# Kernel tuning notes

Measured on AMD Instinct MI355X. Metric: run time of the kernel, lower is better.

The kernel has to match this reference:

```python
import jax, jax.numpy as jnp
import numpy as np

COST_CLASS = 1.0
COST_MASK = 1.0
COST_DICE = 1.0


def setup_inputs() -> dict:
    key = jax.random.key(0)
    k1, k2, k3, k4 = jax.random.split(key, 4)
    B, Q, T, H, W, C = 4, 100, 20, 128, 128, 80
    out_probs = jax.random.normal(k1, (B, Q, C), dtype=jnp.float32)
    out_masks = jax.random.uniform(k2, (B, Q, H, W), dtype=jnp.float32)
    target_masks = jax.random.uniform(k3, (B, T, H, W), dtype=jnp.float32)
    target_labels = jax.random.randint(k4, (B, T), 0, C, dtype=jnp.int64)
    return {"out_probs": out_probs, "out_masks": out_masks,
            "target_masks": target_masks, "target_labels": target_labels}


def reference(out_probs, out_masks, target_masks, target_labels):
    # out_probs: [B,Q,C]; out_masks: [B,Q,H,W]; target_masks: [B,T,H,W]; target_labels: [B,T]
    B, Q = out_probs.shape[:2]
    T = target_labels.shape[1]

    # Classification cost: -softmax(out_probs)[b, q, target_labels[b, t]] -> [B,Q,T]
    prob = jax.nn.softmax(out_probs, axis=-1)
    idx = jnp.broadcast_to(target_labels[:, None, :], (B, Q, T))
    cost_class = -jnp.take_along_axis(prob, idx, axis=2)

    out_flat = out_masks.reshape(B, Q, -1)      # [B,Q,HW]
    tgt_flat = target_masks.reshape(B, T, -1)   # [B,T,HW]

    # Pairwise L1 cost over pixels: [B,Q,T]
    cost_mask = jnp.abs(out_flat[:, :, None, :] - tgt_flat[:, None, :, :]).sum(-1)

    # Pairwise dice cost: numerator via batched matmul, sums broadcast.
    inter = jnp.einsum('bqn,btn->bqt', out_flat, tgt_flat)
    denom = out_flat.sum(-1)[:, :, None] + tgt_flat.sum(-1)[:, None, :]
    cost_dice = 1.0 - (2.0 * inter + 1.0) / (denom + 1.0)

    C_mat = COST_MASK * cost_mask + COST_CLASS * cost_class + COST_DICE * cost_dice
    return C_mat  # [B,Q,T] cost matrix (Hungarian assignment runs on CPU outside)
```

## Files before the change

### kernel.cpp

```cpp
#include <hip/hip_runtime.h>
#include <hip/hip_bf16.h>
#include <math.h>

#define B_ 4
#define Q_ 100
#define T_ 20
#define C_ 80
#define HW_ 16384

#define S_ 16
#define QG_ 4
#define GPB_ (Q_ / QG_)
#define GROUPS_ (B_ * GPB_)
#define SEG4_ (HW_ / S_ / 4)
#define NITER_ (SEG4_ / 64)
#define TW_ 5
#define SUBS_ 4
#define QREC_ 41
#define REC_ (QG_ * QREC_ * SUBS_)
#define GWS_OFF ((size_t)GROUPS_ * S_ * REC_)

typedef float f32x4 __attribute__((ext_vector_type(4)));

__device__ __forceinline__ f32x4 ldnt(const f32x4* p) {
    return __builtin_nontemporal_load(p);
}

__device__ __forceinline__ float wave_reduce4(float v) {
    v += __shfl_down(v, 32);
    v += __shfl_down(v, 16);
    v += __shfl_down(v, 8);
    v += __shfl_down(v, 4);
    return v;
}

template <bool WITH_G>
__device__ __forceinline__ void partial_body(const f32x4* __restrict__ o4,
                                             const f32x4* __restrict__ g4,
                                             float* __restrict__ rec,
                                             float* __restrict__ grec,
                                             int lane, int wave) {
    const int t0 = wave * TW_;

    float accL[QG_][TW_];
    float accI[QG_][TW_];
    float osum[QG_];
    float gsum[TW_];
#pragma unroll
    for (int qi = 0; qi < QG_; ++qi) {
        osum[qi] = 0.f;
#pragma unroll
        for (int tj = 0; tj < TW_; ++tj) { accL[qi][tj] = 0.f; accI[qi][tj] = 0.f; }
    }
#pragma unroll
    for (int tj = 0; tj < TW_; ++tj) gsum[tj] = 0.f;

    const f32x4* op = o4 + lane;
    const f32x4* gp = g4 + (size_t)t0 * (HW_ / 4) + lane;

    f32x4 oc[QG_], gc[TW_], on[QG_], gn[TW_];
#pragma unroll
    for (int qi = 0; qi < QG_; ++qi) oc[qi] = ldnt(op + (size_t)qi * (HW_ / 4));
#pragma unroll
    for (int tj = 0; tj < TW_; ++tj) gc[tj] = gp[(size_t)tj * (HW_ / 4)];

#pragma unroll
    for (int it = 0; it < NITER_; ++it) {
        if (it + 1 < NITER_) {
            const int ofs = (it + 1) * 64;
#pragma unroll
            for (int qi = 0; qi < QG_; ++qi) on[qi] = ldnt(op + (size_t)qi * (HW_ / 4) + ofs);
#pragma unroll
            for (int tj = 0; tj < TW_; ++tj) gn[tj] = gp[(size_t)tj * (HW_ / 4) + ofs];
        }
#pragma unroll
        for (int qi = 0; qi < QG_; ++qi)
            osum[qi] += (oc[qi].x + oc[qi].y) + (oc[qi].z + oc[qi].w);
#pragma unroll
        for (int tj = 0; tj < TW_; ++tj) {
            const f32x4 g = gc[tj];
            if (WITH_G) gsum[tj] += (g.x + g.y) + (g.z + g.w);
#pragma unroll
            for (int qi = 0; qi < QG_; ++qi) {
                const f32x4 o = oc[qi];
                accL[qi][tj] += (fabsf(o.x - g.x) + fabsf(o.y - g.y)) +
                                (fabsf(o.z - g.z) + fabsf(o.w - g.w));
                accI[qi][tj] = fmaf(o.x, g.x, accI[qi][tj]);
                accI[qi][tj] = fmaf(o.y, g.y, accI[qi][tj]);
                accI[qi][tj] = fmaf(o.z, g.z, accI[qi][tj]);
                accI[qi][tj] = fmaf(o.w, g.w, accI[qi][tj]);
            }
        }
        if (it + 1 < NITER_) {
#pragma unroll
            for (int qi = 0; qi < QG_; ++qi) oc[qi] = on[qi];
#pragma unroll
            for (int tj = 0; tj < TW_; ++tj) gc[tj] = gn[tj];
        }
    }

#pragma unroll
    for (int qi = 0; qi < QG_; ++qi) {
#pragma unroll
        for (int tj = 0; tj < TW_; ++tj) {
            const float vL = wave_reduce4(accL[qi][tj]);
            const float vI = wave_reduce4(accI[qi][tj]);
            if (lane < SUBS_) {
                rec[(qi * QREC_ + (t0 + tj)) * SUBS_ + lane]      = vL;
                rec[(qi * QREC_ + 20 + (t0 + tj)) * SUBS_ + lane] = vI;
            }
        }
        const float vo = wave_reduce4(osum[qi]);
        if (wave == 0 && lane < SUBS_) rec[(qi * QREC_ + 40) * SUBS_ + lane] = vo;
    }
    if (WITH_G) {
#pragma unroll
        for (int tj = 0; tj < TW_; ++tj) {
            const float vg = wave_reduce4(gsum[tj]);
            if (lane < SUBS_) grec[(t0 + tj) * SUBS_ + lane] = vg;
        }
    }
}

__global__ __launch_bounds__(256) void partial_kernel(const float* __restrict__ outm,
                                                      const float* __restrict__ tgtm,
                                                      float* __restrict__ ws) {
    const int r = blockIdx.x & 7;
    const int m = blockIdx.x >> 3;
    const int b = r >> 1;
    const int l = m * 2 + (r & 1);
    const int grp_local = l >> 4;
    const int seg = l & (S_ - 1);
    const int qbase = grp_local * QG_;
    const int grp = b * GPB_ + grp_local;

    const int lane = threadIdx.x & 63;
    const int wave = threadIdx.x >> 6;

    const f32x4* o4 = (const f32x4*)(outm + ((size_t)b * Q_ + qbase) * HW_) + seg * SEG4_;
    const f32x4* g4 = (const f32x4*)(tgtm + (size_t)b * T_ * HW_) + seg * SEG4_;
    float* rec  = ws + (size_t)(grp * S_ + seg) * REC_;
    float* grec = ws + GWS_OFF + (size_t)(b * S_ + seg) * T_ * SUBS_;

    if (grp_local == 0) partial_body<true>(o4, g4, rec, grec, lane, wave);
    else                partial_body<false>(o4, g4, rec, grec, lane, wave);
}

__global__ __launch_bounds__(64) void finalize_kernel(const float* __restrict__ probs,
                                                      const int*   __restrict__ labels,
                                                      const float* __restrict__ ws,
                                                      float* __restrict__ out) {
    const int bq = blockIdx.x;
    const int b = bq / Q_;
    const int q = bq % Q_;
    const int grp = b * GPB_ + q / QG_;
    const int qi  = q % QG_;

    __shared__ float s_logit[C_];
    for (int c = threadIdx.x; c < C_; c += 64)
        s_logit[c] = probs[(size_t)bq * C_ + c];
    __syncthreads();

    const int t = threadIdx.x;
    if (t < T_) {
        float L = 0.f, I = 0.f, os = 0.f, ts = 0.f;
#pragma unroll
        for (int s = 0; s < S_; ++s) {
            const float4* r4 = (const float4*)(ws + (size_t)(grp * S_ + s) * REC_);
            const float4* d4 = (const float4*)(ws + GWS_OFF + (size_t)(b * S_ + s) * T_ * SUBS_);
            const float4 a = r4[qi * QREC_ + t];
            const float4 v = r4[qi * QREC_ + 20 + t];
            const float4 c = r4[qi * QREC_ + 40];
            const float4 d = d4[t];
            L  += (a.x + a.y) + (a.z + a.w);
            I  += (v.x + v.y) + (v.z + v.w);
            os += (c.x + c.y) + (c.z + c.w);
            ts += (d.x + d.y) + (d.z + d.w);
        }
        float mx = -INFINITY;
#pragma unroll
        for (int c = 0; c < C_; ++c) mx = fmaxf(mx, s_logit[c]);
        float sum = 0.f;
#pragma unroll
        for (int c = 0; c < C_; ++c) sum += __expf(s_logit[c] - mx);
        const int lab = labels[b * T_ + t];
        const float p = __expf(s_logit[lab] - mx) / sum;

        const float denom = os + ts;
        const float dice = 1.f - (2.f * I + 1.f) / (denom + 1.f);

        out[(size_t)bq * T_ + t] = L - p + dice;
    }
}

extern "C" void kernel_launch(void* const* d_in, const int* in_sizes, int n_in,
                              void* d_out, int out_size, void* d_ws, size_t ws_size,
                              hipStream_t stream) {
    const float* out_probs     = (const float*)d_in[0];
    const float* out_masks     = (const float*)d_in[1];
    const float* target_masks  = (const float*)d_in[2];
    const int*   target_labels = (const int*)d_in[3];
    float* out = (float*)d_out;

    float* partials = (float*)d_ws;

    partial_kernel<<<GROUPS_ * S_, 256, 0, stream>>>(out_masks, target_masks, partials);
    finalize_kernel<<<B_ * Q_, 64, 0, stream>>>(out_probs, target_labels, partials, out);
}
```

Measured before the change: 37.29 us.

## Stage target-mask chunks into double-buffered LDS via global_load_lds

Target-mask tiles are no longer loaded into per-wave registers. They are copied asynchronously straight into a double-buffered shared-memory array with the global_load_lds builtin. Waves stage rows cooperatively and each wave then reads its own 5 rows from LDS. The aim is to cut register pressure from the gc/gn prefetch registers and overlap target fetches with compute. The cost is a block-wide barrier every iteration, plus reliance on the builtin's uniform-LDS-base addressing matching the per-lane destination layout.

```diff
diff --git a/kernel.cpp b/kernel.cpp
--- a/kernel.cpp
+++ b/kernel.cpp
@@ -13,7 +13,8 @@
 #define GPB_ (Q_ / QG_)
 #define GROUPS_ (B_ * GPB_)
 #define SEG4_ (HW_ / S_ / 4)
-#define NITER_ (SEG4_ / 64)
+#define CH_ 64
+#define NITER_ (SEG4_ / CH_)
 #define TW_ 5
 #define SUBS_ 4
 #define QREC_ 41
@@ -24,6 +25,13 @@
 
 __device__ __forceinline__ f32x4 ldnt(const f32x4* p) {
     return __builtin_nontemporal_load(p);
+}
+
+__device__ __forceinline__ void stage16(const f32x4* gsrc, f32x4* ldst) {
+    __builtin_amdgcn_global_load_lds(
+        (const __attribute__((address_space(1))) void*)gsrc,
+        (__attribute__((address_space(3))) void*)ldst,
+        16, 0, 0);
 }
 
 __device__ __forceinline__ float wave_reduce4(float v) {
@@ -37,6 +45,7 @@
 template <bool WITH_G>
 __device__ __forceinline__ void partial_body(const f32x4* __restrict__ o4,
                                              const f32x4* __restrict__ g4,
+                                             f32x4* __restrict__ lbuf,
                                              float* __restrict__ rec,
                                              float* __restrict__ grec,
                                              int lane, int wave) {
@@ -55,30 +64,36 @@
 #pragma unroll
     for (int tj = 0; tj < TW_; ++tj) gsum[tj] = 0.f;
 
-    const f32x4* op = o4 + lane;
-    const f32x4* gp = g4 + (size_t)t0 * (HW_ / 4) + lane;
-
-    f32x4 oc[QG_], gc[TW_], on[QG_], gn[TW_];
-#pragma unroll
-    for (int qi = 0; qi < QG_; ++qi) oc[qi] = ldnt(op + (size_t)qi * (HW_ / 4));
-#pragma unroll
-    for (int tj = 0; tj < TW_; ++tj) gc[tj] = gp[(size_t)tj * (HW_ / 4)];
+#pragma unroll
+    for (int k = 0; k < 5; ++k) {
+        const int t = wave + 4 * k;
+        stage16(g4 + (size_t)t * (HW_ / 4), lbuf + t * CH_ + lane);
+    }
+    f32x4 oc[QG_], on[QG_];
+#pragma unroll
+    for (int qi = 0; qi < QG_; ++qi) oc[qi] = ldnt(o4 + (size_t)qi * (HW_ / 4));
+    __syncthreads();
 
 #pragma unroll
     for (int it = 0; it < NITER_; ++it) {
+        const f32x4* cbuf = lbuf + (it & 1) * (T_ * CH_);
         if (it + 1 < NITER_) {
-            const int ofs = (it + 1) * 64;
-#pragma unroll
-            for (int qi = 0; qi < QG_; ++qi) on[qi] = ldnt(op + (size_t)qi * (HW_ / 4) + ofs);
-#pragma unroll
-            for (int tj = 0; tj < TW_; ++tj) gn[tj] = gp[(size_t)tj * (HW_ / 4) + ofs];
+            f32x4* nbuf = lbuf + ((it + 1) & 1) * (T_ * CH_);
+#pragma unroll
+            for (int k = 0; k < 5; ++k) {
+                const int t = wave + 4 * k;
+                stage16(g4 + (size_t)t * (HW_ / 4) + (it + 1) * CH_, nbuf + t * CH_ + lane);
+            }
+#pragma unroll
+            for (int qi = 0; qi < QG_; ++qi)
+                on[qi] = ldnt(o4 + (size_t)qi * (HW_ / 4) + (it + 1) * CH_);
         }
 #pragma unroll
         for (int qi = 0; qi < QG_; ++qi)
             osum[qi] += (oc[qi].x + oc[qi].y) + (oc[qi].z + oc[qi].w);
 #pragma unroll
         for (int tj = 0; tj < TW_; ++tj) {
-            const f32x4 g = gc[tj];
+            const f32x4 g = cbuf[(t0 + tj) * CH_ + lane];
             if (WITH_G) gsum[tj] += (g.x + g.y) + (g.z + g.w);
 #pragma unroll
             for (int qi = 0; qi < QG_; ++qi) {
@@ -91,11 +106,10 @@
                 accI[qi][tj] = fmaf(o.w, g.w, accI[qi][tj]);
             }
         }
+        __syncthreads();
         if (it + 1 < NITER_) {
 #pragma unroll
             for (int qi = 0; qi < QG_; ++qi) oc[qi] = on[qi];
-#pragma unroll
-            for (int tj = 0; tj < TW_; ++tj) gc[tj] = gn[tj];
         }
     }
 
@@ -125,6 +139,8 @@
 __global__ __launch_bounds__(256) void partial_kernel(const float* __restrict__ outm,
                                                       const float* __restrict__ tgtm,
                                                       float* __restrict__ ws) {
+    __shared__ f32x4 lbuf[2][T_ * CH_];
+
     const int r = blockIdx.x & 7;
     const int m = blockIdx.x >> 3;
     const int b = r >> 1;
@@ -137,13 +153,13 @@
     const int lane = threadIdx.x & 63;
     const int wave = threadIdx.x >> 6;
 
-    const f32x4* o4 = (const f32x4*)(outm + ((size_t)b * Q_ + qbase) * HW_) + seg * SEG4_;
-    const f32x4* g4 = (const f32x4*)(tgtm + (size_t)b * T_ * HW_) + seg * SEG4_;
+    const f32x4* o4 = (const f32x4*)(outm + ((size_t)b * Q_ + qbase) * HW_) + seg * SEG4_ + lane;
+    const f32x4* g4 = (const f32x4*)(tgtm + (size_t)b * T_ * HW_) + seg * SEG4_ + lane;
     float* rec  = ws + (size_t)(grp * S_ + seg) * REC_;
     float* grec = ws + GWS_OFF + (size_t)(b * S_ + seg) * T_ * SUBS_;
 
-    if (grp_local == 0) partial_body<true>(o4, g4, rec, grec, lane, wave);
-    else                partial_body<false>(o4, g4, rec, grec, lane, wave);
+    if (grp_local == 0) partial_body<true>(o4, g4, &lbuf[0][0], rec, grec, lane, wave);
+    else                partial_body<false>(o4, g4, &lbuf[0][0], rec, grec, lane, wave);
 }
 
 __global__ __launch_bounds__(64) void finalize_kernel(const float* __restrict__ probs,
```

Result: slower. 47.10 us (+26.3%).
